# Kernel optimization log

Measured on AMD Instinct MI355X. Metric: run time of the kernel, lower is better.

Reference implementation:

```python
import jax, jax.numpy as jnp
import numpy as np

BS, SEQ, H = 256, 512, 768


def setup_inputs() -> dict:
    key = jax.random.key(0)
    k1, k2, k3, k4, k5 = jax.random.split(key, 5)
    tokens = jax.random.normal(k1, (BS, SEQ, H), dtype=jnp.float32)
    cls_output = jax.random.normal(k2, (BS, H), dtype=jnp.float32)
    # leading-ones attention masks with random valid lengths in [1, SEQ]
    lengths = jax.random.randint(k3, (BS,), 1, SEQ + 1)
    attention_mask = (jnp.arange(SEQ)[None, :] < lengths[:, None]).astype(jnp.int32)
    # additive-attention params (AttentionLayer(hidden_size))
    W = jax.random.normal(k4, (2 * H, H), dtype=jnp.float32) * (1.0 / np.sqrt(2 * H)).astype(np.float32)
    b = jnp.zeros((H,), dtype=jnp.float32)
    v = jax.random.normal(k5, (H,), dtype=jnp.float32) * (1.0 / np.sqrt(H)).astype(np.float32)
    return {"tokens": tokens, "cls_output": cls_output, "attention_mask": attention_mask,
            "W": W, "b": b, "v": v}


def _sample_indices(attention_mask, h):
    # valid length = number of LEADING ones (original breaks at first 0)
    valid = jnp.cumprod(attention_mask, axis=1)            # [bs, seq]
    lengths = jnp.sum(valid, axis=1)                       # [bs]
    # torch.multinomial(uniform, h, replacement=True) == uniform randint in [0, length)
    key = jax.random.key(42)
    u = jax.random.uniform(key, (attention_mask.shape[0], h), dtype=jnp.float32)
    idx = jnp.floor(u * lengths[:, None].astype(jnp.float32)).astype(jnp.int32)
    idx = jnp.minimum(idx, jnp.maximum(lengths[:, None] - 1, 0))
    return idx


def reference(tokens, cls_output, attention_mask, W, b, v):
    bs, seq, h = tokens.shape
    idx = _sample_indices(attention_mask, h)               # [bs, h]
    # embraced[b, j] = tokens[b, idx[b, j], j]
    embraced = jnp.take_along_axis(tokens, idx[:, None, :], axis=1)[:, 0, :]  # [bs, h]
    # additive attention over the pair {cls, embraced}, queried by cls
    cand = jnp.stack([cls_output, embraced], axis=1)       # [bs, 2, h]
    q = jnp.broadcast_to(cls_output[:, None, :], cand.shape)
    energy = jnp.tanh(jnp.concatenate([q, cand], axis=-1) @ W + b) @ v  # [bs, 2]
    alpha = jax.nn.softmax(energy, axis=1)
    return jnp.einsum('bk,bkh->bh', alpha, cand)           # [bs, h]
```

## Files before the change

### kernel.cpp

```cpp
#include <hip/hip_runtime.h>
#include <math.h>

#define BS  256
#define SEQ 512
#define H   768

__device__ __forceinline__ unsigned rotl32(unsigned x, int r) {
  return (x << r) | (x >> (32 - r));
}

__device__ __forceinline__ void threefry_0_42(unsigned& x0, unsigned& x1) {
  const unsigned ks0 = 0u;
  const unsigned ks1 = 42u;
  const unsigned ks2 = ks0 ^ ks1 ^ 0x1BD11BDAu;
  x0 += ks0; x1 += ks1;
#define TF_ROUND(r) { x0 += x1; x1 = rotl32(x1, (r)); x1 ^= x0; }
  TF_ROUND(13) TF_ROUND(15) TF_ROUND(26) TF_ROUND(6)
  x0 += ks1; x1 += ks2 + 1u;
  TF_ROUND(17) TF_ROUND(29) TF_ROUND(16) TF_ROUND(24)
  x0 += ks2; x1 += ks0 + 2u;
  TF_ROUND(13) TF_ROUND(15) TF_ROUND(26) TF_ROUND(6)
  x0 += ks0; x1 += ks1 + 3u;
  TF_ROUND(17) TF_ROUND(29) TF_ROUND(16) TF_ROUND(24)
  x0 += ks1; x1 += ks2 + 4u;
  TF_ROUND(13) TF_ROUND(15) TF_ROUND(26) TF_ROUND(6)
  x0 += ks2; x1 += ks0 + 5u;
#undef TF_ROUND
}

__global__ __launch_bounds__(256) void prep_kernel(
    const float* __restrict__ tokens,
    const int*   __restrict__ mask,
    float* __restrict__ emb,
    float* __restrict__ ge0,
    float* __restrict__ ge1)
{
  const int b = blockIdx.x;
  const int t = threadIdx.x;

  __shared__ int s_len;
  if (t == 0) { s_len = SEQ; ge0[b] = 0.0f; ge1[b] = 0.0f; }
  __syncthreads();

  {
    if (mask[b * SEQ + t] == 0)       atomicMin(&s_len, t);
    if (mask[b * SEQ + t + 256] == 0) atomicMin(&s_len, t + 256);
  }
  __syncthreads();
  const int len = s_len;
  const float lenf = (float)len;

#pragma unroll
  for (int p = 0; p < 3; ++p) {
    const int j = t + 256 * p;
    const unsigned n = (unsigned)(b * H + j);
    unsigned x0 = 0u, x1 = n;
    threefry_0_42(x0, x1);
    const unsigned bits = x0 ^ x1;
    const float u = __uint_as_float((bits >> 9) | 0x3f800000u) - 1.0f;
    int idx = (int)floorf(u * lenf);
    idx = min(idx, len - 1);
    emb[n] = tokens[(size_t)b * (SEQ * H) + (size_t)idx * H + j];
  }
}

#define TM 32
#define TN 32
#define BKK 32
#define PAD 2
__global__ __launch_bounds__(256) void gemm_fused_kernel(
    const float* __restrict__ cls,
    const float* __restrict__ emb,
    const float* __restrict__ W,
    const float* __restrict__ bias,
    const float* __restrict__ v,
    float* __restrict__ ge0,
    float* __restrict__ ge1)
{
  __shared__ float s_c [BKK][TM + PAD];
  __shared__ float s_e [BKK][TM + PAD];
  __shared__ float s_wt[BKK][TN + PAD];
  __shared__ float s_wb[BKK][TN + PAD];

  const int n0 = blockIdx.x * TN;
  const int m0 = blockIdx.y * TM;
  const int t  = threadIdx.x;
  const int tx = t & 15;
  const int ty = t >> 4;

  const float* __restrict__ Wt = W;
  const float* __restrict__ Wb = W + (size_t)H * H;

  float aT[2][2] = {};
  float a0[2][2] = {};
  float a1[2][2] = {};

  const int lk = t & 31, lr = t >> 5;

  for (int kk = 0; kk < H; kk += BKK) {
#pragma unroll
    for (int p = 0; p < 4; ++p) {
      const int r = lr + 8 * p;
      s_c[lk][r]  = cls[(size_t)(m0 + r) * H + kk + lk];
      s_e[lk][r]  = emb[(size_t)(m0 + r) * H + kk + lk];
      s_wt[r][lk] = Wt[(size_t)(kk + r) * H + n0 + lk];
      s_wb[r][lk] = Wb[(size_t)(kk + r) * H + n0 + lk];
    }
    __syncthreads();
#pragma unroll
    for (int k = 0; k < BKK; ++k) {
      const float2 c  = *(const float2*)&s_c [k][2 * ty];
      const float2 e  = *(const float2*)&s_e [k][2 * ty];
      const float2 wt = *(const float2*)&s_wt[k][2 * tx];
      const float2 wb = *(const float2*)&s_wb[k][2 * tx];
      aT[0][0] = fmaf(c.x, wt.x, aT[0][0]);
      aT[0][1] = fmaf(c.x, wt.y, aT[0][1]);
      aT[1][0] = fmaf(c.y, wt.x, aT[1][0]);
      aT[1][1] = fmaf(c.y, wt.y, aT[1][1]);
      a0[0][0] = fmaf(c.x, wb.x, a0[0][0]);
      a0[0][1] = fmaf(c.x, wb.y, a0[0][1]);
      a0[1][0] = fmaf(c.y, wb.x, a0[1][0]);
      a0[1][1] = fmaf(c.y, wb.y, a0[1][1]);
      a1[0][0] = fmaf(e.x, wb.x, a1[0][0]);
      a1[0][1] = fmaf(e.x, wb.y, a1[0][1]);
      a1[1][0] = fmaf(e.y, wb.x, a1[1][0]);
      a1[1][1] = fmaf(e.y, wb.y, a1[1][1]);
    }
    __syncthreads();
  }

  float p0[2] = {0.0f, 0.0f};
  float p1[2] = {0.0f, 0.0f};
#pragma unroll
  for (int j = 0; j < 2; ++j) {
    const int n = n0 + 2 * tx + j;
    const float bb = bias[n];
    const float vv = v[n];
#pragma unroll
    for (int i = 0; i < 2; ++i) {
      p0[i] += vv * tanhf(aT[i][j] + a0[i][j] + bb);
      p1[i] += vv * tanhf(aT[i][j] + a1[i][j] + bb);
    }
  }
#pragma unroll
  for (int off = 8; off > 0; off >>= 1) {
#pragma unroll
    for (int i = 0; i < 2; ++i) {
      p0[i] += __shfl_down(p0[i], off);
      p1[i] += __shfl_down(p1[i], off);
    }
  }
  if (tx == 0) {
#pragma unroll
    for (int i = 0; i < 2; ++i) {
      atomicAdd(&ge0[m0 + 2 * ty + i], p0[i]);
      atomicAdd(&ge1[m0 + 2 * ty + i], p1[i]);
    }
  }
}

__global__ __launch_bounds__(256) void blend_kernel(
    const float* __restrict__ cls,
    const float* __restrict__ emb,
    const float* __restrict__ ge0,
    const float* __restrict__ ge1,
    float* __restrict__ out)
{
  const int b = blockIdx.x;
  const int t = threadIdx.x;

  __shared__ float s_a0, s_a1;
  if (t == 0) {
    const float e0 = ge0[b], e1 = ge1[b];
    const float mx = fmaxf(e0, e1);
    const float x0 = expf(e0 - mx), x1 = expf(e1 - mx);
    const float inv = 1.0f / (x0 + x1);
    s_a0 = x0 * inv; s_a1 = x1 * inv;
  }
  __syncthreads();
  const float a0 = s_a0, a1 = s_a1;
#pragma unroll
  for (int p = 0; p < 3; ++p) {
    const int j = t + 256 * p;
    out[b * H + j] = a0 * cls[b * H + j] + a1 * emb[b * H + j];
  }
}

extern "C" void kernel_launch(void* const* d_in, const int* in_sizes, int n_in,
                              void* d_out, int out_size, void* d_ws, size_t ws_size,
                              hipStream_t stream) {
  const float* tokens = (const float*)d_in[0];
  const float* cls    = (const float*)d_in[1];
  const int*   mask   = (const int*)  d_in[2];
  const float* W      = (const float*)d_in[3];
  const float* bias   = (const float*)d_in[4];
  const float* v      = (const float*)d_in[5];
  float* out = (float*)d_out;

  float* ws  = (float*)d_ws;
  float* emb = ws;
  float* ge0 = ws + BS * H;
  float* ge1 = ge0 + BS;

  prep_kernel<<<BS, 256, 0, stream>>>(tokens, mask, emb, ge0, ge1);

  dim3 g(H / TN, BS / TM);
  gemm_fused_kernel<<<g, 256, 0, stream>>>(cls, emb, W, bias, v, ge0, ge1);

  blend_kernel<<<BS, 256, 0, stream>>>(cls, emb, ge0, ge1, out);
}
```

Before: 495.8 us.

## Fuse blend into GEMM via last-block counter and use wave-shuffle length reduction

Removes the separate blend kernel. Each row-tile of the GEMM increments a per-tile counter, and the last column block to arrive computes the softmax weights and writes the blended output with float4 loads and stores. The prep kernel also replaces the shared-memory atomicMin length search with a wave shuffle min reduction and zeroes the counters. This saves one kernel launch and its scheduling gap, at the cost of threadfence and atomic overhead plus a serialized tail inside the last block of each row tile.

```diff
diff --git a/kernel.cpp b/kernel.cpp
--- a/kernel.cpp
+++ b/kernel.cpp
@@ -33,21 +33,25 @@
     const int*   __restrict__ mask,
     float* __restrict__ emb,
     float* __restrict__ ge0,
-    float* __restrict__ ge1)
+    float* __restrict__ ge1,
+    int*   __restrict__ cnt)
 {
   const int b = blockIdx.x;
   const int t = threadIdx.x;
 
-  __shared__ int s_len;
-  if (t == 0) { s_len = SEQ; ge0[b] = 0.0f; ge1[b] = 0.0f; }
-  __syncthreads();
-
-  {
-    if (mask[b * SEQ + t] == 0)       atomicMin(&s_len, t);
-    if (mask[b * SEQ + t + 256] == 0) atomicMin(&s_len, t + 256);
-  }
-  __syncthreads();
-  const int len = s_len;
+  if (t == 0) { ge0[b] = 0.0f; ge1[b] = 0.0f; }
+  if (b == 0 && t < 8) cnt[t] = 0;
+
+  int cand = SEQ;
+  if (mask[b * SEQ + t] == 0)       cand = t;
+  if (mask[b * SEQ + t + 256] == 0) cand = min(cand, t + 256);
+#pragma unroll
+  for (int off = 32; off > 0; off >>= 1)
+    cand = min(cand, __shfl_xor(cand, off));
+  __shared__ int s_w[4];
+  if ((t & 63) == 0) s_w[t >> 6] = cand;
+  __syncthreads();
+  const int len = min(min(s_w[0], s_w[1]), min(s_w[2], s_w[3]));
   const float lenf = (float)len;
 
 #pragma unroll
@@ -75,7 +79,9 @@
     const float* __restrict__ bias,
     const float* __restrict__ v,
     float* __restrict__ ge0,
-    float* __restrict__ ge1)
+    float* __restrict__ ge1,
+    int*   __restrict__ cnt,
+    float* __restrict__ out)
 {
   __shared__ float s_c [BKK][TM + PAD];
   __shared__ float s_e [BKK][TM + PAD];
@@ -156,33 +162,40 @@
       atomicAdd(&ge0[m0 + 2 * ty + i], p0[i]);
       atomicAdd(&ge1[m0 + 2 * ty + i], p1[i]);
     }
-  }
-}
-
-__global__ __launch_bounds__(256) void blend_kernel(
-    const float* __restrict__ cls,
-    const float* __restrict__ emb,
-    const float* __restrict__ ge0,
-    const float* __restrict__ ge1,
-    float* __restrict__ out)
-{
-  const int b = blockIdx.x;
-  const int t = threadIdx.x;
-
-  __shared__ float s_a0, s_a1;
-  if (t == 0) {
-    const float e0 = ge0[b], e1 = ge1[b];
+    __threadfence();
+  }
+  __syncthreads();
+
+  __shared__ int s_last;
+  if (t == 0) s_last = atomicAdd(&cnt[blockIdx.y], 1);
+  __syncthreads();
+  if (s_last != (H / TN) - 1) return;
+
+  __shared__ float s_a0v[TM], s_a1v[TM];
+  if (t < TM) {
+    const float e0 = atomicAdd(&ge0[m0 + t], 0.0f);
+    const float e1 = atomicAdd(&ge1[m0 + t], 0.0f);
     const float mx = fmaxf(e0, e1);
     const float x0 = expf(e0 - mx), x1 = expf(e1 - mx);
     const float inv = 1.0f / (x0 + x1);
-    s_a0 = x0 * inv; s_a1 = x1 * inv;
-  }
-  __syncthreads();
-  const float a0 = s_a0, a1 = s_a1;
-#pragma unroll
-  for (int p = 0; p < 3; ++p) {
-    const int j = t + 256 * p;
-    out[b * H + j] = a0 * cls[b * H + j] + a1 * emb[b * H + j];
+    s_a0v[t] = x0 * inv;
+    s_a1v[t] = x1 * inv;
+  }
+  __syncthreads();
+
+  for (int q = t; q < TM * (H / 4); q += 256) {
+    const int r  = q / (H / 4);
+    const int c4 = q - r * (H / 4);
+    const size_t base = (size_t)(m0 + r) * H + 4 * c4;
+    const float4 cv = *(const float4*)&cls[base];
+    const float4 ev = *(const float4*)&emb[base];
+    const float a0r = s_a0v[r], a1r = s_a1v[r];
+    float4 o;
+    o.x = a0r * cv.x + a1r * ev.x;
+    o.y = a0r * cv.y + a1r * ev.y;
+    o.z = a0r * cv.z + a1r * ev.z;
+    o.w = a0r * cv.w + a1r * ev.w;
+    *(float4*)&out[base] = o;
   }
 }
 
@@ -201,11 +214,10 @@
   float* emb = ws;
   float* ge0 = ws + BS * H;
   float* ge1 = ge0 + BS;
-
-  prep_kernel<<<BS, 256, 0, stream>>>(tokens, mask, emb, ge0, ge1);
+  int*   cnt = (int*)(ge1 + BS);
+
+  prep_kernel<<<BS, 256, 0, stream>>>(tokens, mask, emb, ge0, ge1, cnt);
 
   dim3 g(H / TN, BS / TM);
-  gemm_fused_kernel<<<g, 256, 0, stream>>>(cls, emb, W, bias, v, ge0, ge1);
-
-  blend_kernel<<<BS, 256, 0, stream>>>(cls, emb, ge0, ge1, out);
-}
+  gemm_fused_kernel<<<g, 256, 0, stream>>>(cls, emb, W, bias, v, ge0, ge1, cnt, out);
+}
```

New measurement: 504.1 us. About the same (+1.7%).
